# Optimization experiments

Hardware: AMD Instinct MI355X
Metric: run time of the kernel (lower is better)

## Reference

```python
import jax, jax.numpy as jnp
import numpy as np

IN_FEATURES = 4096
OUT_FEATURES = 16384
I8_MAX = 127.0
I8_MIN = -128.0


def setup_inputs() -> dict:
    key = jax.random.key(0)
    kx, kw, kb = jax.random.split(key, 3)
    x = jax.random.normal(kx, (2, 4096, IN_FEATURES), dtype=jnp.float32)
    # Original nn.Linear weight [out, in]; QuantLinear stores W.T as int8 [in, out]
    w = jax.random.normal(kw, (OUT_FEATURES, IN_FEATURES), dtype=jnp.float32) * 0.02
    wt = w.T  # [in, out]
    # per-output-channel scale: max_abs over axis=0 of W.T, divided by int8 max
    weight_scale = jnp.max(jnp.abs(wt), axis=0) / I8_MAX  # [out]
    weight_q = jnp.clip(jnp.round(wt / weight_scale[None, :]), I8_MIN, I8_MAX).astype(jnp.int8)
    bias = jax.random.normal(kb, (OUT_FEATURES,), dtype=jnp.float32) * 0.02
    return {"x": x, "weight_q": weight_q, "weight_scale": weight_scale, "bias": bias}


def reference(x, weight_q, weight_scale, bias):
    # flatten leading dims -> [M, in]
    x2 = x.reshape(-1, x.shape[-1])
    # dynamic per-token activation quantization (input_scale is None in module)
    x_scale = jnp.max(jnp.abs(x2), axis=-1, keepdims=True) / I8_MAX  # [M, 1]
    x_scale = jnp.maximum(x_scale, jnp.float32(1e-12))
    x_q = jnp.clip(jnp.round(x2 / x_scale), I8_MIN, I8_MAX)  # integer-valued f32
    # scaled int8 GEMM + dequant (accumulate in f32; values exactly representable)
    acc = jnp.matmul(x_q, weight_q.astype(jnp.float32))  # [M, out]
    out = acc * x_scale * weight_scale[None, :] + bias[None, :]
    return out.reshape(*x.shape[:-1], weight_q.shape[1])
```

## Files before the change

### kernel.cpp

```cpp
#include <hip/hip_runtime.h>
#include <cstdint>
#include <cstddef>

#define IN_F  4096
#define OUT_F 16384
#define NROWS 8192
#define NKT   64

typedef __attribute__((ext_vector_type(4)))  int int32x4;
typedef __attribute__((ext_vector_type(16))) int int32x16;

__device__ __forceinline__ void gload_lds16(const void* g, void* s) {
    __builtin_amdgcn_global_load_lds((const __attribute__((address_space(1))) void*)g,
                                     (__attribute__((address_space(3))) void*)s,
                                     16, 0, 0);
}


__global__ __launch_bounds__(256) void transpose_kernel(const int* __restrict__ w,
                                                        uint8_t* __restrict__ wtS) {
    __shared__ uint8_t tile[64][68];
    const int t  = threadIdx.x;
    const int nb = blockIdx.x * 64;
    const int kt = blockIdx.y;
    const int kb = kt * 64;

#pragma unroll
    for (int p = 0; p < 4; ++p) {
        const int r = p * 16 + (t >> 4);
        const int c4 = t & 15;
        int4 u = *reinterpret_cast<const int4*>(w + (size_t)(kb + r) * OUT_F + nb + c4 * 4);
        uint32_t packed = (uint32_t)(u.x & 255) | ((uint32_t)(u.y & 255) << 8)
                        | ((uint32_t)(u.z & 255) << 16) | ((uint32_t)(u.w & 255) << 24);
        *reinterpret_cast<uint32_t*>(&tile[r][c4 * 4]) = packed;
    }
    __syncthreads();

    const int col = t >> 2;
    const int c   = t & 3;
    uint4 o;
    uint32_t* op = reinterpret_cast<uint32_t*>(&o);
#pragma unroll
    for (int j = 0; j < 4; ++j) {
        const int kk = c * 16 + j * 4;
        op[j] = (uint32_t)tile[kk][col] | ((uint32_t)tile[kk + 1][col] << 8)
              | ((uint32_t)tile[kk + 2][col] << 16) | ((uint32_t)tile[kk + 3][col] << 24);
    }
    const int ntile = nb >> 8;
    const int colg  = (nb & 255) + col;
    *reinterpret_cast<uint4*>(wtS + (((size_t)ntile * NKT + kt) * 4 + c) * 4096 + colg * 16) = o;
}

__global__ __launch_bounds__(256) void quant_kernel(const float* __restrict__ x,
                                                    uint8_t* __restrict__ xqS,
                                                    float* __restrict__ xs) {
    const int t = threadIdx.x;
    const int w = t >> 6, l = t & 63;
    const int half = l >> 5, lh = l & 31;
    const int m = blockIdx.x * 8 + w * 2 + half;
    const float* xr = x + (size_t)m * IN_F;

    float am = 0.0f;
#pragma unroll 8
    for (int jj = 0; jj < 32; ++jj) {
        float4 v = reinterpret_cast<const float4*>(xr)[jj * 32 + lh];
        am = fmaxf(am, fmaxf(fmaxf(fabsf(v.x), fabsf(v.y)),
                             fmaxf(fabsf(v.z), fabsf(v.w))));
    }
#pragma unroll
    for (int off = 16; off; off >>= 1) am = fmaxf(am, __shfl_xor(am, off));

    const float scale = fmaxf(am / 127.0f, 1e-12f);
    if (lh == 0) xs[m] = scale;

    const int mtile = m >> 8, mrow = m & 255;
    uint8_t* ob = xqS + (size_t)mtile * (NKT * 16384) + (size_t)mrow * 16;
#pragma unroll
    for (int j = 0; j < 8; ++j) {
        const int k0 = lh * 128 + j * 16;
        const float4* vp = reinterpret_cast<const float4*>(xr + k0);
        uint4 pk;
        uint32_t* pp = reinterpret_cast<uint32_t*>(&pk);
#pragma unroll
        for (int q = 0; q < 4; ++q) {
            float4 v = vp[q];
            float r0 = fminf(127.f, fmaxf(-128.f, rintf(v.x / scale)));
            float r1 = fminf(127.f, fmaxf(-128.f, rintf(v.y / scale)));
            float r2 = fminf(127.f, fmaxf(-128.f, rintf(v.z / scale)));
            float r3 = fminf(127.f, fmaxf(-128.f, rintf(v.w / scale)));
            pp[q] = ((uint32_t)((int)r0 & 255)) | ((uint32_t)((int)r1 & 255) << 8)
                  | ((uint32_t)((int)r2 & 255) << 16) | ((uint32_t)((int)r3 & 255) << 24);
        }
        const int ktk = k0 >> 6;
        const int c   = (k0 >> 4) & 3;
        *reinterpret_cast<uint4*>(ob + ((size_t)ktk * 4 + c) * 4096) = pk;
    }
}

#define GEMM_STEP(KT, BC, BNX)                                                        \
    {                                                                                 \
        const int q  = ((KT) & 3) * 16384;                                            \
        const int q1 = (((KT) + 1) & 3) * 16384;                                      \
        const int q3 = (((KT) + 3) & 3) * 16384;                                      \
        if ((KT) < NKT - 1) {     \
            const uint8_t* bsrc = bBase + (size_t)((KT) + 1) * 16384 + bOff;          \
            BNX[0] = *reinterpret_cast<const int32x4*>(bsrc);                         \
            BNX[1] = *reinterpret_cast<const int32x4*>(bsrc + 512);                   \
            BNX[2] = *reinterpret_cast<const int32x4*>(bsrc + 8192);                  \
            BNX[3] = *reinterpret_cast<const int32x4*>(bsrc + 8704);                  \
        }                                                                             \
        _Pragma("unroll")            \
        for (int mr = 0; mr < 4; ++mr)                                                \
            af1[mr] = *reinterpret_cast<const int32x4*>(ldsA + q + 8192 + aRd0 + mr * 512); \
        if ((KT) < NKT - 3) {        \
            _Pragma("unroll")                                                         \
            for (int L = 0; L < 2; ++L)                                               \
                gload_lds16(aBase + (size_t)((KT) + 3) * 16384 + L * 8192 + t16,      \
                            ldsA + q3 + L * 8192 + wofs);                             \
        }                                                                             \
        __builtin_amdgcn_s_setprio(1);                                                \
        _Pragma("unroll")                                                             \
        for (int mr = 0; mr < 4; ++mr) {                                              \
            acc[mr][0] = __builtin_amdgcn_mfma_i32_32x32x32_i8(af0[mr], BC[0], acc[mr][0], 0, 0, 0); \
            acc[mr][1] = __builtin_amdgcn_mfma_i32_32x32x32_i8(af0[mr], BC[1], acc[mr][1], 0, 0, 0); \
        }                                                                             \
        __builtin_amdgcn_s_setprio(0);                                                \
        if ((KT) < NKT - 1) {                                                         \
            asm volatile("s_waitcnt lgkmcnt(0)" ::: "memory");         \
            asm volatile("s_waitcnt vmcnt(8)" ::: "memory");    \
            __builtin_amdgcn_s_barrier();                                             \
            __builtin_amdgcn_sched_barrier(0);                                        \
            _Pragma("unroll")      \
            for (int mr = 0; mr < 4; ++mr)                                            \
                af0[mr] = *reinterpret_cast<const int32x4*>(ldsA + q1 + aRd0 + mr * 512); \
        }                                                                             \
        __builtin_amdgcn_s_setprio(1);                                                \
        _Pragma("unroll")                                                             \
        for (int mr = 0; mr < 4; ++mr) {                                              \
            acc[mr][0] = __builtin_amdgcn_mfma_i32_32x32x32_i8(af1[mr], BC[2], acc[mr][0], 0, 0, 0); \
            acc[mr][1] = __builtin_amdgcn_mfma_i32_32x32x32_i8(af1[mr], BC[3], acc[mr][1], 0, 0, 0); \
        }                                                                             \
        __builtin_amdgcn_s_setprio(0);                                                \
    }

__global__ __launch_bounds__(512, 2) void gemm_kernel(const uint8_t* __restrict__ xqS,
                                                      const uint8_t* __restrict__ wtS,
                                                      const float* __restrict__ xs,
                                                      const float* __restrict__ wsc,
                                                      const float* __restrict__ bias,
                                                      float* __restrict__ out) {
    __shared__ uint8_t ldsA[65536];

    const int t    = threadIdx.x;
    const int lane = t & 63;
    const int wid  = t >> 6;
    const int wm   = wid >> 2, wn = wid & 3;

    int bid = blockIdx.x;
    bid = (bid & 7) * 256 + (bid >> 3);
    const int mt = bid >> 6;
    const int nt = bid & 63;

    const uint8_t* aBase = xqS + (size_t)mt * (NKT * 16384);
    const uint8_t* bBase = wtS + (size_t)nt * (NKT * 16384);
    const int t16  = t * 16;
    const int wofs = wid * 1024;

    const int aRd0 = (lane >> 5) * 4096 + wm * 2048 + (lane & 31) * 16;
    const int bOff = (lane >> 5) * 4096 + wn * 1024 + (lane & 31) * 16;

    int32x16 acc[4][2] = {};
    int32x4 af0[4], af1[4], bfA[4], bfB[4];

#pragma unroll
    for (int tt = 0; tt < 3; ++tt)
#pragma unroll
        for (int L = 0; L < 2; ++L)
            gload_lds16(aBase + tt * 16384 + L * 8192 + t16, ldsA + tt * 16384 + L * 8192 + wofs);
    {
        const uint8_t* bsrc = bBase + bOff;
        bfA[0] = *reinterpret_cast<const int32x4*>(bsrc);
        bfA[1] = *reinterpret_cast<const int32x4*>(bsrc + 512);
        bfA[2] = *reinterpret_cast<const int32x4*>(bsrc + 8192);
        bfA[3] = *reinterpret_cast<const int32x4*>(bsrc + 8704);
    }
    asm volatile("s_waitcnt vmcnt(8)" ::: "memory");
    __builtin_amdgcn_s_barrier();
    __builtin_amdgcn_sched_barrier(0);
#pragma unroll
    for (int mr = 0; mr < 4; ++mr)
        af0[mr] = *reinterpret_cast<const int32x4*>(ldsA + aRd0 + mr * 512);

    for (int kt2 = 0; kt2 < NKT; kt2 += 2) {
        GEMM_STEP(kt2,     bfA, bfB);
        GEMM_STEP(kt2 + 1, bfB, bfA);
    }

    const int row0 = mt * 256 + wm * 128;
    const int col0 = nt * 256 + wn * 64;
#pragma unroll
    for (int mr = 0; mr < 4; ++mr) {
        const int rbase = row0 + mr * 32 + 4 * (lane >> 5);
        float xsv[16];
#pragma unroll
        for (int g = 0; g < 16; ++g)
            xsv[g] = xs[rbase + (g & 3) + 8 * (g >> 2)];
#pragma unroll
        for (int nr = 0; nr < 2; ++nr) {
            const int n = col0 + nr * 32 + (lane & 31);
            const float ws_n = wsc[n];
            const float b_n  = bias[n];
#pragma unroll
            for (int g = 0; g < 16; ++g) {
                const int m = rbase + (g & 3) + 8 * (g >> 2);
                out[(size_t)m * OUT_F + n] = (float)acc[mr][nr][g] * xsv[g] * ws_n + b_n;
            }
        }
    }
}

extern "C" void kernel_launch(void* const* d_in, const int* in_sizes, int n_in,
                              void* d_out, int out_size, void* d_ws, size_t ws_size,
                              hipStream_t stream) {
    const float* x    = (const float*)d_in[0];
    const int*   wq   = (const int*)d_in[1];
    const float* wsc  = (const float*)d_in[2];
    const float* bias = (const float*)d_in[3];
    float* out = (float*)d_out;

    uint8_t* ws  = (uint8_t*)d_ws;
    uint8_t* wtS = ws;
    uint8_t* xqS = ws + (size_t)IN_F * OUT_F;
    float*   xs  = (float*)(ws + (size_t)IN_F * OUT_F + (size_t)NROWS * IN_F);

    transpose_kernel<<<dim3(OUT_F / 64, IN_F / 64), 256, 0, stream>>>(wq, wtS);
    quant_kernel<<<NROWS / 8, 256, 0, stream>>>(x, xqS, xs);
    gemm_kernel<<<(NROWS / 256) * (OUT_F / 256), 512, 0, stream>>>(xqS, wtS, xs, wsc, bias, out);
}
```

Before: 782.2 us.

## Prefetch B fragments two k-tiles ahead and regroup block-to-XCD tile mapping

B fragments, which are loaded directly from global memory into registers, are now fetched two k-steps ahead instead of one. The load is issued after the second MFMA group and lands in the buffer that just finished being used, so global latency gets more cover. The vmcnt waits are adjusted to account for the extra outstanding loads. The block-index swizzle is also changed so each XCD owns four consecutive M-tiles while iterating over N, which changes L2 reuse of A versus B. More in-flight loads may add register pressure, and the hand-tuned vmcnt counts have to match the actual instruction order.

```diff
diff --git a/kernel.cpp b/kernel.cpp
--- a/kernel.cpp
+++ b/kernel.cpp
@@ -97,50 +97,56 @@
     }
 }
 
-#define GEMM_STEP(KT, BC, BNX)                                                        \
+#define GEMM_STEP(KT, BSET)                                                           \
     {                                                                                 \
         const int q  = ((KT) & 3) * 16384;                                            \
         const int q1 = (((KT) + 1) & 3) * 16384;                                      \
         const int q3 = (((KT) + 3) & 3) * 16384;                                      \
-        if ((KT) < NKT - 1) {     \
-            const uint8_t* bsrc = bBase + (size_t)((KT) + 1) * 16384 + bOff;          \
-            BNX[0] = *reinterpret_cast<const int32x4*>(bsrc);                         \
-            BNX[1] = *reinterpret_cast<const int32x4*>(bsrc + 512);                   \
-            BNX[2] = *reinterpret_cast<const int32x4*>(bsrc + 8192);                  \
-            BNX[3] = *reinterpret_cast<const int32x4*>(bsrc + 8704);                  \
-        }                                                                             \
-        _Pragma("unroll")            \
+        _Pragma("unroll")           \
         for (int mr = 0; mr < 4; ++mr)                                                \
             af1[mr] = *reinterpret_cast<const int32x4*>(ldsA + q + 8192 + aRd0 + mr * 512); \
-        if ((KT) < NKT - 3) {        \
+        if ((KT) < NKT - 3) {      \
+            const size_t src3 = (size_t)((KT) + 3) * 16384;                           \
             _Pragma("unroll")                                                         \
             for (int L = 0; L < 2; ++L)                                               \
-                gload_lds16(aBase + (size_t)((KT) + 3) * 16384 + L * 8192 + t16,      \
-                            ldsA + q3 + L * 8192 + wofs);                             \
-        }                                                                             \
+                gload_lds16(aBase + src3 + L * 8192 + t16, ldsA + q3 + L * 8192 + wofs); \
+        }                                                                             \
+                                                                      \
         __builtin_amdgcn_s_setprio(1);                                                \
         _Pragma("unroll")                                                             \
         for (int mr = 0; mr < 4; ++mr) {                                              \
-            acc[mr][0] = __builtin_amdgcn_mfma_i32_32x32x32_i8(af0[mr], BC[0], acc[mr][0], 0, 0, 0); \
-            acc[mr][1] = __builtin_amdgcn_mfma_i32_32x32x32_i8(af0[mr], BC[1], acc[mr][1], 0, 0, 0); \
+            acc[mr][0] = __builtin_amdgcn_mfma_i32_32x32x32_i8(af0[mr], BSET[0], acc[mr][0], 0, 0, 0); \
+            acc[mr][1] = __builtin_amdgcn_mfma_i32_32x32x32_i8(af0[mr], BSET[1], acc[mr][1], 0, 0, 0); \
         }                                                                             \
         __builtin_amdgcn_s_setprio(0);                                                \
         if ((KT) < NKT - 1) {                                                         \
-            asm volatile("s_waitcnt lgkmcnt(0)" ::: "memory");         \
-            asm volatile("s_waitcnt vmcnt(8)" ::: "memory");    \
+                 \
+                       \
+            asm volatile("s_waitcnt lgkmcnt(0)" ::: "memory");                        \
+            if ((KT) < NKT - 3)       asm volatile("s_waitcnt vmcnt(12)" ::: "memory"); \
+            else if ((KT) == NKT - 3) asm volatile("s_waitcnt vmcnt(10)" ::: "memory"); \
+            else                      asm volatile("s_waitcnt vmcnt(8)" ::: "memory");  \
             __builtin_amdgcn_s_barrier();                                             \
             __builtin_amdgcn_sched_barrier(0);                                        \
-            _Pragma("unroll")      \
+            _Pragma("unroll")     \
             for (int mr = 0; mr < 4; ++mr)                                            \
                 af0[mr] = *reinterpret_cast<const int32x4*>(ldsA + q1 + aRd0 + mr * 512); \
         }                                                                             \
+                                                                      \
         __builtin_amdgcn_s_setprio(1);                                                \
         _Pragma("unroll")                                                             \
         for (int mr = 0; mr < 4; ++mr) {                                              \
-            acc[mr][0] = __builtin_amdgcn_mfma_i32_32x32x32_i8(af1[mr], BC[2], acc[mr][0], 0, 0, 0); \
-            acc[mr][1] = __builtin_amdgcn_mfma_i32_32x32x32_i8(af1[mr], BC[3], acc[mr][1], 0, 0, 0); \
+            acc[mr][0] = __builtin_amdgcn_mfma_i32_32x32x32_i8(af1[mr], BSET[2], acc[mr][0], 0, 0, 0); \
+            acc[mr][1] = __builtin_amdgcn_mfma_i32_32x32x32_i8(af1[mr], BSET[3], acc[mr][1], 0, 0, 0); \
         }                                                                             \
         __builtin_amdgcn_s_setprio(0);                                                \
+        if ((KT) < NKT - 2) {   \
+            const uint8_t* bsrc = bBase + (size_t)((KT) + 2) * 16384 + bGo;           \
+            BSET[0] = *reinterpret_cast<const int32x4*>(bsrc);                        \
+            BSET[1] = *reinterpret_cast<const int32x4*>(bsrc + 512);                  \
+            BSET[2] = *reinterpret_cast<const int32x4*>(bsrc + 8192);                 \
+            BSET[3] = *reinterpret_cast<const int32x4*>(bsrc + 8704);                 \
+        }                                                                             \
     }
 
 __global__ __launch_bounds__(512, 2) void gemm_kernel(const uint8_t* __restrict__ xqS,
@@ -156,10 +162,10 @@
     const int wid  = t >> 6;
     const int wm   = wid >> 2, wn = wid & 3;
 
-    int bid = blockIdx.x;
-    bid = (bid & 7) * 256 + (bid >> 3);
-    const int mt = bid >> 6;
-    const int nt = bid & 63;
+    const int xcd = blockIdx.x & 7;
+    const int i   = blockIdx.x >> 3;
+    const int mt  = xcd * 4 + (i & 3);
+    const int nt  = i >> 2;
 
     const uint8_t* aBase = xqS + (size_t)mt * (NKT * 16384);
     const uint8_t* bBase = wtS + (size_t)nt * (NKT * 16384);
@@ -167,10 +173,10 @@
     const int wofs = wid * 1024;
 
     const int aRd0 = (lane >> 5) * 4096 + wm * 2048 + (lane & 31) * 16;
-    const int bOff = (lane >> 5) * 4096 + wn * 1024 + (lane & 31) * 16;
+    const int bGo  = (lane >> 5) * 4096 + wn * 1024 + (lane & 31) * 16;
 
     int32x16 acc[4][2] = {};
-    int32x4 af0[4], af1[4], bfA[4], bfB[4];
+    int32x4 af0[4], af1[4], bE[4], bO[4];
 
 #pragma unroll
     for (int tt = 0; tt < 3; ++tt)
@@ -178,22 +184,28 @@
         for (int L = 0; L < 2; ++L)
             gload_lds16(aBase + tt * 16384 + L * 8192 + t16, ldsA + tt * 16384 + L * 8192 + wofs);
     {
-        const uint8_t* bsrc = bBase + bOff;
-        bfA[0] = *reinterpret_cast<const int32x4*>(bsrc);
-        bfA[1] = *reinterpret_cast<const int32x4*>(bsrc + 512);
-        bfA[2] = *reinterpret_cast<const int32x4*>(bsrc + 8192);
-        bfA[3] = *reinterpret_cast<const int32x4*>(bsrc + 8704);
-    }
-    asm volatile("s_waitcnt vmcnt(8)" ::: "memory");
+        const uint8_t* b0 = bBase + bGo;
+        const uint8_t* b1 = bBase + 16384 + bGo;
+        bE[0] = *reinterpret_cast<const int32x4*>(b0);
+        bE[1] = *reinterpret_cast<const int32x4*>(b0 + 512);
+        bE[2] = *reinterpret_cast<const int32x4*>(b0 + 8192);
+        bE[3] = *reinterpret_cast<const int32x4*>(b0 + 8704);
+        bO[0] = *reinterpret_cast<const int32x4*>(b1);
+        bO[1] = *reinterpret_cast<const int32x4*>(b1 + 512);
+        bO[2] = *reinterpret_cast<const int32x4*>(b1 + 8192);
+        bO[3] = *reinterpret_cast<const int32x4*>(b1 + 8704);
+    }
+    asm volatile("s_waitcnt vmcnt(12)" ::: "memory");
     __builtin_amdgcn_s_barrier();
     __builtin_amdgcn_sched_barrier(0);
+
 #pragma unroll
     for (int mr = 0; mr < 4; ++mr)
         af0[mr] = *reinterpret_cast<const int32x4*>(ldsA + aRd0 + mr * 512);
 
     for (int kt2 = 0; kt2 < NKT; kt2 += 2) {
-        GEMM_STEP(kt2,     bfA, bfB);
-        GEMM_STEP(kt2 + 1, bfB, bfA);
+        GEMM_STEP(kt2,     bE);
+        GEMM_STEP(kt2 + 1, bO);
     }
 
     const int row0 = mt * 256 + wm * 128;
```

After: 782.4 us. About the same (+0.0%).
